# Kernel optimization log

Hardware: AMD Instinct MI355X
Metric: run time of the kernel (lower is better)

The kernel has to match this reference:

```python
import jax, jax.numpy as jnp
import numpy as np

N_NODES = 100000


def gcn_conv(x, src, dst, W, b):
    # x: [N, F_in]; src/dst: [E'] (self-loops already appended)
    n = x.shape[0]
    deg = jax.ops.segment_sum(jnp.ones_like(src, dtype=x.dtype), dst, num_segments=n)
    dinv = jnp.where(deg > 0, jax.lax.rsqrt(deg), 0.0)
    norm = dinv[src] * dinv[dst]                      # [E']
    h = x @ W                                         # [N, F_out] (GEMM first: F_out small)
    msg = h[src] * norm[:, None]                      # gather + scale
    out = jax.ops.segment_sum(msg, dst, num_segments=n)  # scatter-add
    return out + b


def setup_inputs() -> dict:
    key = jax.random.key(0)
    k1, k2, k3, k4 = jax.random.split(key, 4)
    x = jax.random.normal(k1, (N_NODES, 1433), dtype=jnp.float32)
    edge_index = jax.random.randint(k2, (2, 3200000), 0, N_NODES, dtype=jnp.int32)
    W1 = jax.random.normal(k3, (1433, 32), dtype=jnp.float32) * (1.0 / np.sqrt(1433.0))
    b1 = jnp.zeros((32,), dtype=jnp.float32)
    W2 = jax.random.normal(k4, (32, 7), dtype=jnp.float32) * (1.0 / np.sqrt(32.0))
    b2 = jnp.zeros((7,), dtype=jnp.float32)
    return {"x": x, "edge_index": edge_index, "W1": W1, "b1": b1, "W2": W2, "b2": b2}


def reference(x, edge_index, W1, b1, W2, b2):
    n = x.shape[0]
    loop = jnp.arange(n, dtype=edge_index.dtype)      # add self-loops (GCNConv default)
    src = jnp.concatenate([edge_index[0], loop])
    dst = jnp.concatenate([edge_index[1], loop])
    h = gcn_conv(x, src, dst, W1, b1)
    h = jax.nn.relu(h)
    # F.dropout with training=False (eval mode) is identity
    h = gcn_conv(h, src, dst, W2, b2)
    return jax.nn.log_softmax(h, axis=1)
```

## Files before the change

kernel.cpp:

```cpp
#include <hip/hip_runtime.h>
#include <math.h>

#define F0 1433
#define F1 32
#define F2 7

__global__ void k_init_deg(float* __restrict__ deg, int N) {
    int i = blockIdx.x * 256 + threadIdx.x;
    if (i < N) deg[i] = 1.0f;
}

__global__ void k_count_deg(const int* __restrict__ dst, float* __restrict__ deg, int E) {
    int e = blockIdx.x * 256 + threadIdx.x;
    if (e < E) atomicAdd(&deg[dst[e]], 1.0f);
}

__global__ void k_dinv(float* __restrict__ deg, int N) {
    int i = blockIdx.x * 256 + threadIdx.x;
    if (i < N) deg[i] = rsqrtf(deg[i]);
}

#define BM 64
#define BK 64
#define XS_LD 68
__global__ __launch_bounds__(256) void k_gemm1(const float* __restrict__ x,
                                               const float* __restrict__ W,
                                               float* __restrict__ h, int N) {
    __shared__ float xs[BM * XS_LD];
    __shared__ float wsm[BK * F1];
    const int tid  = threadIdx.x;
    const int row0 = blockIdx.x * BM;
    const int cg   = tid & 7;
    const int r    = tid >> 3;

    float acc0x = 0.f, acc0y = 0.f, acc0z = 0.f, acc0w = 0.f;
    float acc1x = 0.f, acc1y = 0.f, acc1z = 0.f, acc1w = 0.f;

    for (int k0 = 0; k0 < F0; k0 += BK) {
        #pragma unroll
        for (int l = 0; l < 16; ++l) {
            int idx = tid + l * 256;
            int i = idx >> 6, j = idx & 63;
            int gr = row0 + i, gk = k0 + j;
            float v = 0.f;
            if (gr < N && gk < F0) v = x[(long)gr * F0 + gk];
            xs[i * XS_LD + j] = v;
        }
        #pragma unroll
        for (int l = 0; l < 8; ++l) {
            int idx = tid + l * 256;
            int kk = idx >> 5;
            int gk = k0 + kk;
            wsm[idx] = (gk < F0) ? W[gk * F1 + (idx & 31)] : 0.f;
        }
        __syncthreads();

        #pragma unroll
        for (int kk = 0; kk < BK; kk += 4) {
            float4 xa = *(const float4*)&xs[r * XS_LD + kk];
            float4 xb = *(const float4*)&xs[(r + 32) * XS_LD + kk];
            const float av[4] = {xa.x, xa.y, xa.z, xa.w};
            const float bv[4] = {xb.x, xb.y, xb.z, xb.w};
            #pragma unroll
            for (int u = 0; u < 4; ++u) {
                float4 w = *(const float4*)&wsm[(kk + u) * F1 + cg * 4];
                float a = av[u], b = bv[u];
                acc0x += a * w.x; acc0y += a * w.y; acc0z += a * w.z; acc0w += a * w.w;
                acc1x += b * w.x; acc1y += b * w.y; acc1z += b * w.z; acc1w += b * w.w;
            }
        }
        __syncthreads();
    }
    int gr0 = row0 + r, gr1 = row0 + r + 32;
    if (gr0 < N) *(float4*)&h[(long)gr0 * F1 + cg * 4] = make_float4(acc0x, acc0y, acc0z, acc0w);
    if (gr1 < N) *(float4*)&h[(long)gr1 * F1 + cg * 4] = make_float4(acc1x, acc1y, acc1z, acc1w);
}

__global__ void k_selfloop1(const float* __restrict__ h1, const float* __restrict__ dinv,
                            float* __restrict__ agg, int N) {
    int t = blockIdx.x * 256 + threadIdx.x;
    if (t < N * F1) {
        int i = t >> 5;
        float d = dinv[i];
        agg[t] = h1[t] * d * d;
    }
}

__global__ void k_scatter1(const int* __restrict__ src, const int* __restrict__ dst,
                           const float* __restrict__ dinv, const float* __restrict__ h1,
                           float* __restrict__ agg, int E) {
    int t = blockIdx.x * 256 + threadIdx.x;
    int e = t >> 5;
    if (e >= E) return;
    int f = t & 31;
    int s = src[e], d = dst[e];
    float w = dinv[s] * dinv[d];
    atomicAdd(&agg[d * F1 + f], h1[s * F1 + f] * w);
}

__global__ __launch_bounds__(256) void k_layer2(const float* __restrict__ agg1,
                                                const float* __restrict__ b1,
                                                const float* __restrict__ W2,
                                                const float* __restrict__ dinv,
                                                float* __restrict__ h2,
                                                float* __restrict__ out, int N) {
    __shared__ float w2s[F1 * F2];
    __shared__ float b1s[F1];
    int tid = threadIdx.x;
    if (tid < F1 * F2) w2s[tid] = W2[tid];
    if (tid < F1) b1s[tid] = b1[tid];
    __syncthreads();
    int i = blockIdx.x * 256 + tid;
    if (i >= N) return;
    float v[F1];
    #pragma unroll
    for (int u = 0; u < 8; ++u) {
        float4 t = *(const float4*)&agg1[(long)i * F1 + u * 4];
        v[u*4+0] = fmaxf(t.x + b1s[u*4+0], 0.f);
        v[u*4+1] = fmaxf(t.y + b1s[u*4+1], 0.f);
        v[u*4+2] = fmaxf(t.z + b1s[u*4+2], 0.f);
        v[u*4+3] = fmaxf(t.w + b1s[u*4+3], 0.f);
    }
    float o[F2] = {0.f, 0.f, 0.f, 0.f, 0.f, 0.f, 0.f};
    #pragma unroll
    for (int k = 0; k < F1; ++k) {
        float a = v[k];
        #pragma unroll
        for (int c = 0; c < F2; ++c) o[c] += a * w2s[k * F2 + c];
    }
    float di = dinv[i];
    float dd = di * di;
    #pragma unroll
    for (int c = 0; c < F2; ++c) {
        h2[(long)i * F2 + c] = o[c];
        out[(long)i * F2 + c] = o[c] * dd;
    }
}

__global__ void k_scatter2(const int* __restrict__ src, const int* __restrict__ dst,
                           const float* __restrict__ dinv, const float* __restrict__ h2,
                           float* __restrict__ out, int E) {
    int t = blockIdx.x * 256 + threadIdx.x;
    int e = t >> 3;
    int c = t & 7;
    if (e >= E || c >= F2) return;
    int s = src[e], d = dst[e];
    float w = dinv[s] * dinv[d];
    atomicAdd(&out[(long)d * F2 + c], h2[(long)s * F2 + c] * w);
}

__global__ void k_logsoftmax(float* __restrict__ out, const float* __restrict__ b2, int N) {
    int i = blockIdx.x * 256 + threadIdx.x;
    if (i >= N) return;
    float v[F2];
    float m = -1e30f;
    #pragma unroll
    for (int c = 0; c < F2; ++c) {
        v[c] = out[(long)i * F2 + c] + b2[c];
        m = fmaxf(m, v[c]);
    }
    float s = 0.f;
    #pragma unroll
    for (int c = 0; c < F2; ++c) s += expf(v[c] - m);
    float l = logf(s);
    #pragma unroll
    for (int c = 0; c < F2; ++c) out[(long)i * F2 + c] = v[c] - m - l;
}

extern "C" void kernel_launch(void* const* d_in, const int* in_sizes, int n_in,
                              void* d_out, int out_size, void* d_ws, size_t ws_size,
                              hipStream_t stream) {
    const float* x  = (const float*)d_in[0];
    const int*   ei = (const int*)d_in[1];
    const float* W1 = (const float*)d_in[2];
    const float* b1 = (const float*)d_in[3];
    const float* W2 = (const float*)d_in[4];
    const float* b2 = (const float*)d_in[5];
    float* out = (float*)d_out;

    const int N = in_sizes[0] / F0;
    const int E = in_sizes[1] / 2;
    const int* src = ei;
    const int* dst = ei + E;

    float* ws   = (float*)d_ws;
    size_t o    = 0;
    float* dinv = ws;        o += (size_t)((N + 3) & ~3);
    float* h1   = ws + o;    o += (size_t)N * F1;
    float* agg1 = ws + o;    o += (size_t)N * F1;
    float* h2   = h1;

    const int nb_N  = (N + 255) / 256;
    const int nb_E  = (E + 255) / 256;

    k_init_deg  <<<nb_N, 256, 0, stream>>>(dinv, N);
    k_count_deg <<<nb_E, 256, 0, stream>>>(dst, dinv, E);
    k_dinv      <<<nb_N, 256, 0, stream>>>(dinv, N);

    k_gemm1     <<<(N + BM - 1) / BM, 256, 0, stream>>>(x, W1, h1, N);

    k_selfloop1 <<<((size_t)N * F1 + 255) / 256, 256, 0, stream>>>(h1, dinv, agg1, N);
    k_scatter1  <<<((size_t)E * 32 + 255) / 256, 256, 0, stream>>>(src, dst, dinv, h1, agg1, E);

    k_layer2    <<<nb_N, 256, 0, stream>>>(agg1, b1, W2, dinv, h2, out, N);

    k_scatter2  <<<((size_t)E * 8 + 255) / 256, 256, 0, stream>>>(src, dst, dinv, h2, out, E);

    k_logsoftmax<<<nb_N, 256, 0, stream>>>(out, b2, N);
}
```

Before: 2.067 ms.

## Register-prefetch GEMM tiles, enlarge row tile, fuse self-loop init into GEMM

The layer-1 GEMM now loads the next K-tile of x and W into registers while computing on the current shared-memory tile, so global loads overlap with compute. The row tile is doubled to 128, giving each thread four output rows. The self-loop initialisation of agg1 is folded into the GEMM epilogue, which removes one kernel and a full reread of h1. This raises register pressure (32 prefetch registers plus 16 accumulators) and uses a launch-bounds occupancy hint, so occupancy may drop.

```diff
diff --git a/kernel.cpp b/kernel.cpp
--- a/kernel.cpp
+++ b/kernel.cpp
@@ -20,69 +20,112 @@
     if (i < N) deg[i] = rsqrtf(deg[i]);
 }
 
-#define BM 64
+#define BM 128
 #define BK 64
 #define XS_LD 68
-__global__ __launch_bounds__(256) void k_gemm1(const float* __restrict__ x,
-                                               const float* __restrict__ W,
-                                               float* __restrict__ h, int N) {
+
+#define STAGE_LOAD(K0)                                                       \
+    {                                                                        \
+        const int gk = (K0) + j;                                             \
+        const bool kok = gk < F0;                                            \
+        const float* xp = x + (long)(row0 + i0) * F0 + gk;                   \
+        if (rowfull) {                                                       \
+            _Pragma("unroll")                                                \
+            for (int l = 0; l < 32; ++l)                                     \
+                px[l] = kok ? xp[(long)(4 * l) * F0] : 0.f;                  \
+        } else {                                                             \
+            _Pragma("unroll")                                                \
+            for (int l = 0; l < 32; ++l) {                                   \
+                int gr = row0 + i0 + 4 * l;                                  \
+                px[l] = (gr < N && kok) ? xp[(long)(4 * l) * F0] : 0.f;      \
+            }                                                                \
+        }                                                                    \
+        _Pragma("unroll")                                                    \
+        for (int l = 0; l < 8; ++l) {                                        \
+            int idx = tid + l * 256;                                         \
+            int gkw = (K0) + (idx >> 5);                                     \
+            pw[l] = (gkw < F0) ? W[gkw * F1 + (idx & 31)] : 0.f;             \
+        }                                                                    \
+    }
+
+#define STAGE_WRITE()                                                        \
+    {                                                                        \
+        _Pragma("unroll")                                                    \
+        for (int l = 0; l < 32; ++l) xs[(i0 + 4 * l) * XS_LD + j] = px[l];   \
+        _Pragma("unroll")                                                    \
+        for (int l = 0; l < 8; ++l) wsm[tid + l * 256] = pw[l];              \
+    }
+
+#define COMPUTE()                                                            \
+    _Pragma("unroll")                                                        \
+    for (int kk = 0; kk < BK; kk += 4) {                                     \
+        float4 x0 = *(const float4*)&xs[(r     ) * XS_LD + kk];              \
+        float4 x1 = *(const float4*)&xs[(r + 32) * XS_LD + kk];              \
+        float4 x2 = *(const float4*)&xs[(r + 64) * XS_LD + kk];              \
+        float4 x3 = *(const float4*)&xs[(r + 96) * XS_LD + kk];              \
+        const float a0[4] = {x0.x, x0.y, x0.z, x0.w};                        \
+        const float a1[4] = {x1.x, x1.y, x1.z, x1.w};                        \
+        const float a2[4] = {x2.x, x2.y, x2.z, x2.w};                        \
+        const float a3[4] = {x3.x, x3.y, x3.z, x3.w};                        \
+        _Pragma("unroll")                                                    \
+        for (int u = 0; u < 4; ++u) {                                        \
+            float4 w = *(const float4*)&wsm[(kk + u) * F1 + cg * 4];         \
+            acc[0][0] += a0[u] * w.x; acc[0][1] += a0[u] * w.y;              \
+            acc[0][2] += a0[u] * w.z; acc[0][3] += a0[u] * w.w;              \
+            acc[1][0] += a1[u] * w.x; acc[1][1] += a1[u] * w.y;              \
+            acc[1][2] += a1[u] * w.z; acc[1][3] += a1[u] * w.w;              \
+            acc[2][0] += a2[u] * w.x; acc[2][1] += a2[u] * w.y;              \
+            acc[2][2] += a2[u] * w.z; acc[2][3] += a2[u] * w.w;              \
+            acc[3][0] += a3[u] * w.x; acc[3][1] += a3[u] * w.y;              \
+            acc[3][2] += a3[u] * w.z; acc[3][3] += a3[u] * w.w;              \
+        }                                                                    \
+    }
+
+__global__ __launch_bounds__(256, 3) void k_gemm1(const float* __restrict__ x,
+                                                  const float* __restrict__ W,
+                                                  const float* __restrict__ dinv,
+                                                  float* __restrict__ h,
+                                                  float* __restrict__ agg, int N) {
     __shared__ float xs[BM * XS_LD];
     __shared__ float wsm[BK * F1];
     const int tid  = threadIdx.x;
     const int row0 = blockIdx.x * BM;
     const int cg   = tid & 7;
     const int r    = tid >> 3;
-
-    float acc0x = 0.f, acc0y = 0.f, acc0z = 0.f, acc0w = 0.f;
-    float acc1x = 0.f, acc1y = 0.f, acc1z = 0.f, acc1w = 0.f;
-
-    for (int k0 = 0; k0 < F0; k0 += BK) {
-        #pragma unroll
-        for (int l = 0; l < 16; ++l) {
-            int idx = tid + l * 256;
-            int i = idx >> 6, j = idx & 63;
-            int gr = row0 + i, gk = k0 + j;
-            float v = 0.f;
-            if (gr < N && gk < F0) v = x[(long)gr * F0 + gk];
-            xs[i * XS_LD + j] = v;
+    const int j    = tid & 63;
+    const int i0   = tid >> 6;
+    const bool rowfull = (row0 + BM <= N);
+
+    float acc[4][4] = {{0.f, 0.f, 0.f, 0.f}, {0.f, 0.f, 0.f, 0.f},
+                       {0.f, 0.f, 0.f, 0.f}, {0.f, 0.f, 0.f, 0.f}};
+    float px[32];
+    float pw[8];
+
+    STAGE_LOAD(0)
+    STAGE_WRITE()
+    __syncthreads();
+
+    const int nt = (F0 + BK - 1) / BK;
+    for (int t = 0; t < nt - 1; ++t) {
+        STAGE_LOAD((t + 1) * BK)
+        COMPUTE()
+        __syncthreads();
+        STAGE_WRITE()
+        __syncthreads();
+    }
+    COMPUTE()
+
+    #pragma unroll
+    for (int m = 0; m < 4; ++m) {
+        int gr = row0 + r + 32 * m;
+        if (gr < N) {
+            float4 o = make_float4(acc[m][0], acc[m][1], acc[m][2], acc[m][3]);
+            *(float4*)&h[(long)gr * F1 + cg * 4] = o;
+            float d = dinv[gr];
+            float dd = d * d;
+            *(float4*)&agg[(long)gr * F1 + cg * 4] =
+                make_float4(o.x * dd, o.y * dd, o.z * dd, o.w * dd);
         }
-        #pragma unroll
-        for (int l = 0; l < 8; ++l) {
-            int idx = tid + l * 256;
-            int kk = idx >> 5;
-            int gk = k0 + kk;
-            wsm[idx] = (gk < F0) ? W[gk * F1 + (idx & 31)] : 0.f;
-        }
-        __syncthreads();
-
-        #pragma unroll
-        for (int kk = 0; kk < BK; kk += 4) {
-            float4 xa = *(const float4*)&xs[r * XS_LD + kk];
-            float4 xb = *(const float4*)&xs[(r + 32) * XS_LD + kk];
-            const float av[4] = {xa.x, xa.y, xa.z, xa.w};
-            const float bv[4] = {xb.x, xb.y, xb.z, xb.w};
-            #pragma unroll
-            for (int u = 0; u < 4; ++u) {
-                float4 w = *(const float4*)&wsm[(kk + u) * F1 + cg * 4];
-                float a = av[u], b = bv[u];
-                acc0x += a * w.x; acc0y += a * w.y; acc0z += a * w.z; acc0w += a * w.w;
-                acc1x += b * w.x; acc1y += b * w.y; acc1z += b * w.z; acc1w += b * w.w;
-            }
-        }
-        __syncthreads();
-    }
-    int gr0 = row0 + r, gr1 = row0 + r + 32;
-    if (gr0 < N) *(float4*)&h[(long)gr0 * F1 + cg * 4] = make_float4(acc0x, acc0y, acc0z, acc0w);
-    if (gr1 < N) *(float4*)&h[(long)gr1 * F1 + cg * 4] = make_float4(acc1x, acc1y, acc1z, acc1w);
-}
-
-__global__ void k_selfloop1(const float* __restrict__ h1, const float* __restrict__ dinv,
-                            float* __restrict__ agg, int N) {
-    int t = blockIdx.x * 256 + threadIdx.x;
-    if (t < N * F1) {
-        int i = t >> 5;
-        float d = dinv[i];
-        agg[t] = h1[t] * d * d;
     }
 }
 
@@ -197,9 +240,8 @@
     k_count_deg <<<nb_E, 256, 0, stream>>>(dst, dinv, E);
     k_dinv      <<<nb_N, 256, 0, stream>>>(dinv, N);
 
-    k_gemm1     <<<(N + BM - 1) / BM, 256, 0, stream>>>(x, W1, h1, N);
-
-    k_selfloop1 <<<((size_t)N * F1 + 255) / 256, 256, 0, stream>>>(h1, dinv, agg1, N);
+    k_gemm1     <<<(N + BM - 1) / BM, 256, 0, stream>>>(x, W1, dinv, h1, agg1, N);
+
     k_scatter1  <<<((size_t)E * 32 + 255) / 256, 256, 0, stream>>>(src, dst, dinv, h1, agg1, E);
 
     k_layer2    <<<nb_N, 256, 0, stream>>>(agg1, b1, W2, dinv, h2, out, N);
```

Result: faster. 1.877 ms (-9.2%).
